# Optimization experiments

Hardware: AMD Instinct MI355X
Metric: run time of the kernel (lower is better)

The kernel has to match this reference:

```python
import jax, jax.numpy as jnp
import numpy as np

B, NQ, NK, C, H = 4, 1024, 1024, 768, 12
DH = C // H
SCALE = DH ** -0.5
EPS = 1e-5  # nn.LayerNorm default
NEG_INF = float('-inf')


def _ln(x, g, b):
    m = jnp.mean(x, axis=-1, keepdims=True)
    v = jnp.mean((x - m) ** 2, axis=-1, keepdims=True)
    return (x - m) * jax.lax.rsqrt(v + EPS) * g + b


def _heads(t):  # [B,N,C] -> [B,H,N,Dh]
    Bq, N, _ = t.shape
    return t.reshape(Bq, N, H, DH).transpose(0, 2, 1, 3)


def setup_inputs() -> dict:
    key = jax.random.key(0)
    ks = jax.random.split(key, 32)
    w = lambda k, shape: jax.random.normal(k, shape, jnp.float32) * 0.02
    g = lambda k: 1.0 + jax.random.normal(k, (C,), jnp.float32) * 0.02
    b = lambda k: jax.random.normal(k, (C,), jnp.float32) * 0.02
    inp = {
        'x': jax.random.normal(ks[0], (B, NQ, C), jnp.float32),
        'y': jax.random.normal(ks[1], (B, NK, C), jnp.float32),
        'xpos': jnp.arange(B * NQ, dtype=jnp.int32).reshape(B, NQ),
        'ypos': jnp.arange(B * NK, dtype=jnp.int32).reshape(B, NK),
        'mask': jax.random.randint(ks[2], (NQ, NK), 0, 2) > 0,
        'similarities': jax.random.normal(ks[3], (B, H, NQ, NK), jnp.float32),
        # norms
        'ln1_g': g(ks[4]), 'ln1_b': b(ks[5]),
        'ln2_g': g(ks[6]), 'ln2_b': b(ks[7]),
        'ln3_g': g(ks[8]), 'ln3_b': b(ks[9]),
        'lny_g': g(ks[10]), 'lny_b': b(ks[11]),
        # self-attn (qkv_bias=False)
        'qkv_w': w(ks[12], (3 * C, C)),
        'aproj_w': w(ks[13], (C, C)), 'aproj_b': b(ks[14]),
        # cross-attn
        'pq_w': w(ks[15], (C, C)), 'pk_w': w(ks[16], (C, C)), 'pv_w': w(ks[17], (C, C)),
        'cproj_w': w(ks[18], (C, C)), 'cproj_b': b(ks[19]),
        # mlp (hidden = 4*C)
        'fc1_w': w(ks[20], (4 * C, C)), 'fc1_b': jax.random.normal(ks[21], (4 * C,), jnp.float32) * 0.02,
        'fc2_w': w(ks[22], (C, 4 * C)), 'fc2_b': b(ks[23]),
    }
    return inp


def reference(x, y, xpos, ypos, mask, similarities,
              ln1_g, ln1_b, ln2_g, ln2_b, ln3_g, ln3_b, lny_g, lny_b,
              qkv_w, aproj_w, aproj_b,
              pq_w, pk_w, pv_w, cproj_w, cproj_b,
              fc1_w, fc1_b, fc2_w, fc2_b):
    # ---- self-attention (rope=None, dropout=0) ----
    xn = _ln(x, ln1_g, ln1_b)
    qkv = (xn @ qkv_w.T).reshape(B, NQ, 3, H, DH).transpose(2, 0, 3, 1, 4)
    q, k, v = qkv[0], qkv[1], qkv[2]                       # [B,H,Nq,Dh]
    attn = jax.nn.softmax(jnp.einsum('bhqd,bhkd->bhqk', q, k) * SCALE, axis=-1)
    sa = jnp.einsum('bhqk,bhkd->bhqd', attn, v).transpose(0, 2, 1, 3).reshape(B, NQ, C)
    x = x + sa @ aproj_w.T + aproj_b

    # ---- sparse cross-attention with similarity bias + mask ----
    y_ = _ln(y, lny_g, lny_b)
    xn2 = _ln(x, ln2_g, ln2_b)
    cq = _heads(xn2 @ pq_w.T)                              # [B,H,Nq,Dh]
    ck = _heads(y_ @ pk_w.T)                               # [B,H,Nk,Dh]
    cv = _heads(y_ @ pv_w.T)
    scores = jnp.einsum('bhqd,bhkd->bhqk', cq, ck) * SCALE
    sims_c = similarities - jnp.mean(similarities, axis=1, keepdims=True)
    scores = scores + sims_c
    scores = jnp.where(mask[None, None], scores, NEG_INF)
    cattn = jax.nn.softmax(scores, axis=-1)
    ca = jnp.einsum('bhqk,bhkd->bhqd', cattn, cv).transpose(0, 2, 1, 3).reshape(B, NQ, C)
    x = x + ca @ cproj_w.T + cproj_b

    # ---- MLP (exact GELU, as nn.GELU default) ----
    xn3 = _ln(x, ln3_g, ln3_b)
    h = jax.nn.gelu(xn3 @ fc1_w.T + fc1_b, approximate=False)
    x = x + h @ fc2_w.T + fc2_b
    return (x, y)
```

## Files before the change

kernel.cpp:

```cpp
#include <hip/hip_runtime.h>
#include <cstdint>
#include <cstddef>


typedef __bf16 bf16;
typedef __attribute__((ext_vector_type(8))) __bf16 bf16x8;
typedef __attribute__((ext_vector_type(4))) __bf16 bf16x4;
typedef __attribute__((ext_vector_type(4))) float f32x4;

typedef __attribute__((address_space(1))) void gvoid;
typedef __attribute__((address_space(3))) void lvoid;

#define DEVI static __device__ __forceinline__

DEVI void gload16(const void* g, void* l) {
  __builtin_amdgcn_global_load_lds((gvoid*)(uintptr_t)g, (lvoid*)(uintptr_t)l, 16, 0, 0);
}

DEVI f32x4 mfma_bf16(bf16x8 a, bf16x8 b, f32x4 c) {
  return __builtin_amdgcn_mfma_f32_16x16x32_bf16(a, b, c, 0, 0, 0);
}


template<int BM, int BN, bool BIAS, bool GELU, bool RES, bool OBF, bool VT>
DEVI void gemm_dev(bf16* As, bf16* Bs, int by, int bx,
                   const bf16* __restrict__ A, const bf16* __restrict__ Bt,
                   const float* __restrict__ bias, const float* __restrict__ res,
                   bf16* __restrict__ Cb, float* __restrict__ Cf,
                   bf16* __restrict__ vtOut, int vtBase, int N, int K)
{
  constexpr int WM = BM / 2, WN = BN / 2;
  constexpr int FM = WM / 16, FN = WN / 16;
  const int tid = threadIdx.x;
  const int lane = tid & 63;
  const int wv = tid >> 6;
  const int wr = wv >> 1, wc = wv & 1;
  const int l15 = lane & 15, lg = lane >> 4;
  const int bm = by * BM, bn = bx * BN;

  f32x4 acc[FM][FN];
  const f32x4 z = {0.f, 0.f, 0.f, 0.f};
  #pragma unroll
  for (int i = 0; i < FM; ++i)
    #pragma unroll
    for (int jj = 0; jj < FN; ++jj) acc[i][jj] = z;

  for (int k0 = 0; k0 < K; k0 += 64) {
    __syncthreads();
    #pragma unroll
    for (int c = tid; c < BM * 8; c += 256) {
      const int row = c >> 3, colb = (c & 7) << 4;
      gload16((const char*)A + ((size_t)(bm + row) * K + k0) * 2 + colb,
              (char*)As + (size_t)c * 16);
    }
    #pragma unroll
    for (int c = tid; c < BN * 8; c += 256) {
      const int row = c >> 3, colb = (c & 7) << 4;
      gload16((const char*)Bt + ((size_t)(bn + row) * K + k0) * 2 + colb,
              (char*)Bs + (size_t)c * 16);
    }
    __syncthreads();
    #pragma unroll
    for (int kk = 0; kk < 64; kk += 32) {
      bf16x8 af[FM], bfr[FN];
      #pragma unroll
      for (int mi = 0; mi < FM; ++mi)
        af[mi] = *(const bf16x8*)(As + (size_t)(wr * WM + mi * 16 + l15) * 64 + kk + lg * 8);
      #pragma unroll
      for (int ni = 0; ni < FN; ++ni)
        bfr[ni] = *(const bf16x8*)(Bs + (size_t)(wc * WN + ni * 16 + l15) * 64 + kk + lg * 8);
      #pragma unroll
      for (int mi = 0; mi < FM; ++mi)
        #pragma unroll
        for (int ni = 0; ni < FN; ++ni)
          acc[mi][ni] = mfma_bf16(af[mi], bfr[ni], acc[mi][ni]);
    }
  }

  #pragma unroll
  for (int mi = 0; mi < FM; ++mi) {
    const int row0 = bm + wr * WM + mi * 16 + lg * 4;
    #pragma unroll
    for (int ni = 0; ni < FN; ++ni) {
      const int col = bn + wc * WN + ni * 16 + l15;
      if constexpr (VT) {
        if (col >= vtBase) {
          const int hd = col - vtBase;
          const int bb = row0 >> 10, n0 = row0 & 1023;
          bf16x4 ov;
          #pragma unroll
          for (int r = 0; r < 4; ++r) ov[r] = (bf16)acc[mi][ni][r];
          *(bf16x4*)(vtOut + ((size_t)(bb * 768 + hd)) * 1024 + n0) = ov;
          continue;
        }
      }
      #pragma unroll
      for (int r = 0; r < 4; ++r) {
        float v = acc[mi][ni][r];
        if constexpr (BIAS) v += bias[col];
        if constexpr (GELU) v = 0.5f * v * (1.0f + erff(v * 0.70710678118654752f));
        if constexpr (RES)  v += res[(size_t)(row0 + r) * N + col];
        if constexpr (OBF)  Cb[(size_t)(row0 + r) * N + col] = (bf16)v;
        else                Cf[(size_t)(row0 + r) * N + col] = v;
      }
    }
  }
}

DEVI void biasr_dev(int blk,
                    const float* __restrict__ sim,
                    const unsigned char* __restrict__ mask,
                    bf16* __restrict__ out)
{
  const int b = blk >> 10, q = blk & 1023;
  const int t = threadIdx.x, lane = t & 63;

  int ds = 0;
  #pragma unroll
  for (int i = 0; i < 4; ++i) {
    const int idx = (lane * 4 + i) * 4;
    ds += mask[idx + 1] + mask[idx + 2] + mask[idx + 3];
  }
  #pragma unroll
  for (int o = 32; o; o >>= 1) ds += __shfl_xor(ds, o);
  const int msh = (ds == 0) ? 2 : 0;

  const int k4 = t * 4;
  const float* sb = sim + (size_t)b * 12 * 1048576;
  f32x4 sv[12];
  f32x4 acc = {0.f, 0.f, 0.f, 0.f};
  #pragma unroll
  for (int h = 0; h < 12; ++h) {
    sv[h] = *(const f32x4*)(sb + ((size_t)h * 1024 + q) * 1024 + k4);
    acc += sv[h];
  }
  const f32x4 mean = acc * (1.0f / 12.0f);

  float mb[4];
  if (msh == 0) {
    const uchar4 mv = *(const uchar4*)(mask + (size_t)q * 1024 + k4);
    mb[0] = mv.x ? 0.f : -1e30f; mb[1] = mv.y ? 0.f : -1e30f;
    mb[2] = mv.z ? 0.f : -1e30f; mb[3] = mv.w ? 0.f : -1e30f;
  } else {
    const int4 mv = *(const int4*)((const int*)mask + (size_t)q * 1024 + k4);
    mb[0] = mv.x ? 0.f : -1e30f; mb[1] = mv.y ? 0.f : -1e30f;
    mb[2] = mv.z ? 0.f : -1e30f; mb[3] = mv.w ? 0.f : -1e30f;
  }

  bf16* ob = out + (size_t)(b * 1024 + q) * 12 * 1024;
  #pragma unroll
  for (int h = 0; h < 12; ++h) {
    bf16x4 o;
    #pragma unroll
    for (int j = 0; j < 4; ++j)
      o[j] = (bf16)(sv[h][j] - mean[j] + mb[j]);
    *(bf16x4*)(ob + h * 1024 + k4) = o;
  }
}

DEVI void lnw_dev(int row,
                  const float* __restrict__ xin, const float* __restrict__ g,
                  const float* __restrict__ be, bf16* __restrict__ out)
{
  const int lane = threadIdx.x & 63;
  const f32x4* xr = (const f32x4*)(xin + (size_t)row * 768);
  f32x4 v[3];
  #pragma unroll
  for (int j = 0; j < 3; ++j) v[j] = xr[lane + 64 * j];
  float s = 0.f;
  #pragma unroll
  for (int j = 0; j < 3; ++j) s += v[j][0] + v[j][1] + v[j][2] + v[j][3];
  #pragma unroll
  for (int o = 32; o; o >>= 1) s += __shfl_xor(s, o);
  const float mean = s * (1.0f / 768.0f);
  float q = 0.f;
  #pragma unroll
  for (int j = 0; j < 3; ++j)
    #pragma unroll
    for (int e = 0; e < 4; ++e) { const float d = v[j][e] - mean; q += d * d; }
  #pragma unroll
  for (int o = 32; o; o >>= 1) q += __shfl_xor(q, o);
  const float inv = rsqrtf(q * (1.0f / 768.0f) + 1e-5f);
  #pragma unroll
  for (int j = 0; j < 3; ++j) {
    const int c = lane + 64 * j;
    const f32x4 gv = ((const f32x4*)g)[c];
    const f32x4 bv = ((const f32x4*)be)[c];
    bf16x4 o4;
    #pragma unroll
    for (int e = 0; e < 4; ++e)
      o4[e] = (bf16)((v[j][e] - mean) * inv * gv[e] + bv[e]);
    *((bf16x4*)out + (size_t)row * 192 + c) = o4;
  }
}


struct CvtArgs {
  const float* src[8];
  bf16* dst[8];
  int end[8];
};

__global__ __launch_bounds__(256)
void prep_k(CvtArgs a,
            const float* __restrict__ x, const float* __restrict__ g1,
            const float* __restrict__ b1, bf16* __restrict__ xn,
            const float* __restrict__ y, const float* __restrict__ gy,
            const float* __restrict__ by_, bf16* __restrict__ yln)
{
  const int f = blockIdx.x;
  const int t = threadIdx.x;
  if (f < 2304) {
    #pragma unroll
    for (int j = 0; j < 4; ++j) {
      const int i = f * 1024 + j * 256 + t;
      int s = 0;
      #pragma unroll
      for (int k = 0; k < 7; ++k) s += (i >= a.end[k]) ? 1 : 0;
      const int base = s ? a.end[s - 1] : 0;
      const int off = i - base;
      const f32x4 v = *((const f32x4*)a.src[s] + off);
      bf16x4 o;
      o[0] = (bf16)v[0]; o[1] = (bf16)v[1]; o[2] = (bf16)v[2]; o[3] = (bf16)v[3];
      *(bf16x4*)(a.dst[s] + (size_t)off * 4) = o;
    }
  } else {
    const int row = (f - 2304) * 4 + (t >> 6);
    if (row < 4096) lnw_dev(row, x, g1, b1, xn);
    else            lnw_dev(row - 4096, y, gy, by_, yln);
  }
}

template<int BM, int BN, bool BIAS, bool GELU, bool RES, bool OBF, bool VT>
__global__ __launch_bounds__(256)
void gemm_bt(const bf16* __restrict__ A, const bf16* __restrict__ Bt,
             const float* __restrict__ bias, const float* __restrict__ res,
             bf16* __restrict__ Cb, float* __restrict__ Cf,
             bf16* __restrict__ vtOut, int vtBase,
             int nyPerXcd, int N, int K,
             int nCompute,
             const float* __restrict__ bsim, const unsigned char* __restrict__ bmask,
             bf16* __restrict__ bout, int bbase)
{
  __shared__ bf16 As[BM * 64];
  __shared__ bf16 Bs[BN * 64];
  const int f = blockIdx.x;
  if (f >= nCompute) {
    biasr_dev(bbase + f - nCompute, bsim, bmask, bout);
    return;
  }
  const int xcd = f & 7, j = f >> 3;
  const int by = xcd + 8 * (j % nyPerXcd);
  const int bx = j / nyPerXcd;
  gemm_dev<BM,BN,BIAS,GELU,RES,OBF,VT>(As, Bs, by, bx,
      A, Bt, bias, res, Cb, Cf, vtOut, vtBase, N, K);
}

__global__ __launch_bounds__(256)
void apkv_k(const bf16* __restrict__ sa, const bf16* __restrict__ w_ap,
            const float* __restrict__ apb, const float* __restrict__ x,
            float* __restrict__ x1,
            const bf16* __restrict__ yln, const bf16* __restrict__ w_pkv,
            bf16* __restrict__ ckv, bf16* __restrict__ cvtT,
            const float* __restrict__ bsim, const unsigned char* __restrict__ bmask,
            bf16* __restrict__ bout, int bbase)
{
  __shared__ bf16 As[128 * 64];
  __shared__ bf16 Bs[128 * 64];
  const int f = blockIdx.x;
  if (f >= 768) {
    biasr_dev(bbase + f - 768, bsim, bmask, bout);
    return;
  }
  if (f < 384) {
    const int xcd = f & 7, j = f >> 3;
    const int by = xcd + 8 * (j % 8);
    const int bx = j / 8;
    gemm_dev<64,128,true,false,true,false,false>(As, Bs, by, bx,
        sa, w_ap, apb, x, nullptr, x1, nullptr, 0, 768, 768);
  } else {
    const int g = f - 384;
    const int xcd = g & 7, j = g >> 3;
    const int by = xcd + 8 * (j % 4);
    const int bx = j / 4;
    gemm_dev<128,128,false,false,false,true,true>(As, Bs, by, bx,
        yln, w_pkv, nullptr, nullptr, ckv, nullptr, cvtT, 768, 1536, 768);
  }
}

__global__ __launch_bounds__(256)
void fc2copy_k(const bf16* __restrict__ hbuf, const bf16* __restrict__ w_f2,
               const float* __restrict__ f2b, const float* __restrict__ x2,
               float* __restrict__ outp,
               const float* __restrict__ y, float* __restrict__ ycopy)
{
  __shared__ bf16 As[128 * 64];
  __shared__ bf16 Bs[128 * 64];
  const int f = blockIdx.x;
  if (f < 384) {
    const int xcd = f & 7, j = f >> 3;
    const int by = xcd + 8 * (j % 8);
    const int bx = j / 8;
    gemm_dev<64,128,true,false,true,false,false>(As, Bs, by, bx,
        hbuf, w_f2, f2b, x2, nullptr, outp, nullptr, 0, 768, 3072);
  } else {
    for (int i = (f - 384) * 256 + threadIdx.x; i < 786432; i += 512 * 256)
      ((f32x4*)ycopy)[i] = ((const f32x4*)y)[i];
  }
}

__global__ __launch_bounds__(256)
void ln_k(const float* __restrict__ xin, const float* __restrict__ g,
          const float* __restrict__ be, bf16* __restrict__ out)
{
  lnw_dev(blockIdx.x * 4 + (threadIdx.x >> 6), xin, g, be, out);
}

template<int CROSS>
__global__ __launch_bounds__(256, 3)
void fattn_k(const bf16* __restrict__ Qp, int ldq,
             const bf16* __restrict__ Kp, int ldk,
             const bf16* __restrict__ Vt,
             const bf16* __restrict__ bias,
             bf16* __restrict__ Out,
             int nCompute,
             const float* __restrict__ bsim, const unsigned char* __restrict__ bmask,
             bf16* __restrict__ bout, int bbase)
{
  __shared__ bf16 Kl[2][64 * 64];
  __shared__ bf16 Vl[2][64 * 64];
  __shared__ bf16 Pl[4][16 * 72];

  const int f = blockIdx.x;
  if (f >= nCompute) {
    biasr_dev(bbase + f - nCompute, bsim, bmask, bout);
    return;
  }
  const int r8 = f & 7, rest = f >> 3;
  const int c6 = rest % 6, qt = rest / 6;
  const int pp = r8 + 8 * c6;
  const int b = pp / 12, hh = pp % 12;
  const int tid = threadIdx.x, lane = tid & 63, wq = tid >> 6;
  const int l15 = lane & 15, lg = lane >> 4;

  bf16x8 qreg0, qreg1;
  {
    const bf16* qsrc = Qp + (size_t)(b * 1024 + qt * 64 + wq * 16 + l15) * ldq + hh * 64 + lg * 8;
    qreg0 = *(const bf16x8*)qsrc;
    qreg1 = *(const bf16x8*)(qsrc + 32);
  }
  const char* Kbase = (const char*)(Kp + (size_t)b * 1024 * ldk + hh * 64);
  const char* Vbase = (const char*)(Vt + (size_t)(b * 12 + hh) * 64 * 1024);
  const bf16* biasRow = nullptr;
  if constexpr (CROSS)
    biasRow = bias + ((size_t)(b * 1024 + qt * 64 + wq * 16 + l15) * 12 + hh) * 1024;

  f32x4 oacc[4];
  const f32x4 z = {0.f, 0.f, 0.f, 0.f};
  #pragma unroll
  for (int i = 0; i < 4; ++i) oacc[i] = z;
  float m_run = -1e30f, l_run = 0.f;

  char* PlW = (char*)&Pl[wq][0];
  const int swz = (l15 & 7) << 4;

  auto stage = [&](int buf, int t) {
    const int k0 = t * 64;
    #pragma unroll
    for (int jj = 0; jj < 2; ++jj) {
      const int c = jj * 256 + tid;
      const int r = c >> 3;
      const int sw = ((c & 7) ^ (r & 7)) << 4;
      gload16(Kbase + ((size_t)(k0 + r) * ldk) * 2 + sw, (char*)&Kl[buf][0] + (size_t)c * 16);
      gload16(Vbase + (size_t)r * 2048 + (size_t)k0 * 2 + sw, (char*)&Vl[buf][0] + (size_t)c * 16);
    }
  };

  stage(0, 0);
  __syncthreads();

  for (int t = 0; t < 16; ++t) {
    const int cur = t & 1;
    const int k0 = t * 64;
    if (t < 15) stage(cur ^ 1, t + 1);

    bf16x4 bv[4];
    if constexpr (CROSS) {
      const bf16* bp = biasRow + k0 + lg * 4;
      #pragma unroll
      for (int ni = 0; ni < 4; ++ni) bv[ni] = *(const bf16x4*)(bp + ni * 16);
    }

    f32x4 sacc[4];
    #pragma unroll
    for (int i = 0; i < 4; ++i) sacc[i] = z;
    #pragma unroll
    for (int ni = 0; ni < 4; ++ni) {
      const int rowb = (ni * 16 + l15) * 128;
      const bf16x8 a0 = *(const bf16x8*)((char*)&Kl[cur][0] + rowb + ((lg * 16) ^ swz));
      const bf16x8 a1 = *(const bf16x8*)((char*)&Kl[cur][0] + rowb + ((64 + lg * 16) ^ swz));
      sacc[ni] = mfma_bf16(a0, qreg0, sacc[ni]);
      sacc[ni] = mfma_bf16(a1, qreg1, sacc[ni]);
    }

    float sv[16];
    #pragma unroll
    for (int ni = 0; ni < 4; ++ni)
      #pragma unroll
      for (int r = 0; r < 4; ++r)
        sv[ni * 4 + r] = sacc[ni][r] * 0.125f;
    if constexpr (CROSS) {
      #pragma unroll
      for (int ni = 0; ni < 4; ++ni)
        #pragma unroll
        for (int r = 0; r < 4; ++r)
          sv[ni * 4 + r] += (float)bv[ni][r];
    }
    float mx = sv[0];
    #pragma unroll
    for (int jj = 1; jj < 16; ++jj) mx = fmaxf(mx, sv[jj]);
    mx = fmaxf(mx, __shfl_xor(mx, 16));
    mx = fmaxf(mx, __shfl_xor(mx, 32));
    const float mnew = fmaxf(m_run, mx);
    const float corr = __expf(m_run - mnew);
    m_run = mnew;
    float ps = 0.f;
    #pragma unroll
    for (int jj = 0; jj < 16; ++jj) { sv[jj] = __expf(sv[jj] - mnew); ps += sv[jj]; }
    l_run = l_run * corr + ps;

    #pragma unroll
    for (int ni = 0; ni < 4; ++ni) {
      bf16x4 pw;
      #pragma unroll
      for (int r = 0; r < 4; ++r) pw[r] = (bf16)sv[ni * 4 + r];
      *(bf16x4*)(PlW + l15 * 144 + ni * 32 + lg * 8) = pw;
    }
    float cr[4];
    #pragma unroll
    for (int r = 0; r < 4; ++r) cr[r] = __shfl(corr, ((lane >> 4) << 2) + r);
    #pragma unroll
    for (int nd = 0; nd < 4; ++nd)
      #pragma unroll
      for (int r = 0; r < 4; ++r) oacc[nd][r] *= cr[r];

    const bf16x8 p0 = *(const bf16x8*)(PlW + l15 * 144 + lg * 16);
    const bf16x8 p1 = *(const bf16x8*)(PlW + l15 * 144 + 64 + lg * 16);
    #pragma unroll
    for (int nd = 0; nd < 4; ++nd) {
      const int rowb = (nd * 16 + l15) * 128;
      const bf16x8 v0 = *(const bf16x8*)((char*)&Vl[cur][0] + rowb + ((lg * 16) ^ swz));
      const bf16x8 v1 = *(const bf16x8*)((char*)&Vl[cur][0] + rowb + ((64 + lg * 16) ^ swz));
      oacc[nd] = mfma_bf16(p0, v0, oacc[nd]);
      oacc[nd] = mfma_bf16(p1, v1, oacc[nd]);
    }
    __syncthreads();
  }

  float ls = l_run + __shfl_xor(l_run, 16);
  ls += __shfl_xor(ls, 32);
  const float inv = 1.0f / ls;
  float ivr[4];
  #pragma unroll
  for (int r = 0; r < 4; ++r) ivr[r] = __shfl(inv, ((lane >> 4) << 2) + r);
  bf16* ob = Out + (size_t)(b * 1024 + qt * 64 + wq * 16 + lg * 4) * 768 + hh * 64 + l15;
  #pragma unroll
  for (int r = 0; r < 4; ++r)
    #pragma unroll
    for (int nd = 0; nd < 4; ++nd)
      ob[(size_t)r * 768 + nd * 16] = (bf16)(oacc[nd][r] * ivr[r]);
}

extern "C" void kernel_launch(void* const* d_in, const int* in_sizes, int n_in,
                              void* d_out, int out_size, void* d_ws, size_t ws_size,
                              hipStream_t stream)
{
  (void)in_sizes; (void)n_in; (void)out_size; (void)ws_size;
  const float* x    = (const float*)d_in[0];
  const float* y    = (const float*)d_in[1];
  const unsigned char* mask = (const unsigned char*)d_in[4];
  const float* sim  = (const float*)d_in[5];
  const float* ln1g = (const float*)d_in[6];
  const float* ln1b = (const float*)d_in[7];
  const float* ln2g = (const float*)d_in[8];
  const float* ln2b = (const float*)d_in[9];
  const float* ln3g = (const float*)d_in[10];
  const float* ln3b = (const float*)d_in[11];
  const float* lnyg = (const float*)d_in[12];
  const float* lnyb = (const float*)d_in[13];
  const float* qkvw = (const float*)d_in[14];
  const float* apw  = (const float*)d_in[15];
  const float* apb  = (const float*)d_in[16];
  const float* pqw  = (const float*)d_in[17];
  const float* pkw  = (const float*)d_in[18];
  const float* pvw  = (const float*)d_in[19];
  const float* cpw  = (const float*)d_in[20];
  const float* cpb  = (const float*)d_in[21];
  const float* f1w  = (const float*)d_in[22];
  const float* f1b  = (const float*)d_in[23];
  const float* f2w  = (const float*)d_in[24];
  const float* f2b  = (const float*)d_in[25];

  char* ws = (char*)d_ws;
  size_t off = 0;
  auto alloc = [&](size_t bytes) -> void* {
    off = (off + 255) & ~(size_t)255;
    void* p = ws + off;
    off += bytes;
    return p;
  };
  const size_t T = 4096;
  bf16* w_qkv = (bf16*)alloc((size_t)2304 * 768 * 2);
  bf16* w_ap  = (bf16*)alloc((size_t)768 * 768 * 2);
  bf16* w_pq  = (bf16*)alloc((size_t)768 * 768 * 2);
  bf16* w_pkv = (bf16*)alloc((size_t)1536 * 768 * 2);
  bf16* w_cp  = (bf16*)alloc((size_t)768 * 768 * 2);
  bf16* w_f1  = (bf16*)alloc((size_t)3072 * 768 * 2);
  bf16* w_f2  = (bf16*)alloc((size_t)768 * 3072 * 2);
  bf16* xn    = (bf16*)alloc(T * 768 * 2);
  bf16* qkvo  = (bf16*)alloc(T * 2304 * 2);
  bf16* vt    = (bf16*)alloc((size_t)48 * 64 * 1024 * 2);
  bf16* sa    = (bf16*)alloc(T * 768 * 2);
  float* x1   = (float*)alloc(T * 768 * 4);
  bf16* yln   = (bf16*)alloc(T * 768 * 2);
  bf16* xn2   = (bf16*)alloc(T * 768 * 2);
  bf16* cqf   = (bf16*)alloc(T * 768 * 2);
  bf16* ckv   = (bf16*)alloc(T * 1536 * 2);
  bf16* cvtT  = (bf16*)alloc((size_t)48 * 64 * 1024 * 2);
  bf16* biasA = (bf16*)alloc((size_t)4 * 1024 * 12 * 1024 * 2);
  bf16* ca    = (bf16*)alloc(T * 768 * 2);
  float* x2   = (float*)alloc(T * 768 * 4);
  bf16* xn3   = (bf16*)alloc(T * 768 * 2);
  bf16* hbuf  = (bf16*)alloc(T * 3072 * 2);

  CvtArgs a;
  {
    const float* srcs[8] = {qkvw, apw, pqw, pkw, pvw, cpw, f1w, f2w};
    bf16* dsts[8] = {w_qkv, w_ap, w_pq, w_pkv, w_pkv + 768 * 768, w_cp, w_f1, w_f2};
    const int n4s[8] = {442368, 147456, 147456, 147456, 147456, 147456, 589824, 589824};
    int cum = 0;
    for (int j = 0; j < 8; ++j) {
      a.src[j] = srcs[j]; a.dst[j] = dsts[j];
      cum += n4s[j]; a.end[j] = cum;
    }
  }

  prep_k<<<4352, 256, 0, stream>>>(a, x, ln1g, ln1b, xn, y, lnyg, lnyb, yln);

  gemm_bt<128,128,false,false,false,true,true><<<1600, 256, 0, stream>>>(
      xn, w_qkv, nullptr, nullptr, qkvo, nullptr, vt, 1536, 4, 2304, 768,
      576, sim, mask, biasA, 0);

  fattn_k<0><<<1792, 256, 0, stream>>>(
      qkvo, 2304, qkvo + 768, 2304, vt, nullptr, sa,
      768, sim, mask, biasA, 1024);

  apkv_k<<<1792, 256, 0, stream>>>(sa, w_ap, apb, x, x1, yln, w_pkv, ckv, cvtT,
                                   sim, mask, biasA, 2048);

  ln_k<<<1024, 256, 0, stream>>>(x1, ln2g, ln2b, xn2);

  gemm_bt<64,128,false,false,false,true,false><<<1408, 256, 0, stream>>>(
      xn2, w_pq, nullptr, nullptr, cqf, nullptr, nullptr, 0, 8, 768, 768,
      384, sim, mask, biasA, 3072);

  fattn_k<1><<<768, 256, 0, stream>>>(
      cqf, 768, ckv, 1536, cvtT, biasA, ca,
      768, sim, mask, biasA, 0);

  gemm_bt<64,128,true,false,true,false,false><<<384, 256, 0, stream>>>(
      ca, w_cp, cpb, x1, nullptr, x2, nullptr, 0, 8, 768, 768,
      384, sim, mask, biasA, 0);

  ln_k<<<1024, 256, 0, stream>>>(x2, ln3g, ln3b, xn3);

  gemm_bt<128,128,true,true,false,true,false><<<768, 256, 0, stream>>>(
      xn3, w_f1, f1b, nullptr, hbuf, nullptr, nullptr, 0, 4, 3072, 768,
      768, sim, mask, biasA, 0);

  fc2copy_k<<<896, 256, 0, stream>>>(
      hbuf, w_f2, f2b, x2, (float*)d_out, y, (float*)d_out + 3145728);
}
```

Before: 349.9 us.

## Spread weight conversion, y-LN and bias prep across compute kernels; coalesce cross-attn bias loads

The prep kernel now converts only the QKV weights and runs LN1. The remaining weight conversions and the y LayerNorm move into spare blocks of the QKV GEMM and self-attention launches, and the similarity-bias blocks are redistributed across launches. In cross-attention, each lane loads 16 contiguous bias values per tile and a per-wave LDS buffer transposes them into the MFMA layout, replacing scattered 4-element loads. The aim is to shorten the serial prep phase by overlapping it with compute and to coalesce the bias reads. The cost is extra LDS traffic and shared memory in the cross-attention kernel, plus added branching in the auxiliary blocks.

```diff
diff --git a/kernel.cpp b/kernel.cpp
--- a/kernel.cpp
+++ b/kernel.cpp
@@ -194,40 +194,62 @@
   }
 }
 
-
-struct CvtArgs {
-  const float* src[8];
-  bf16* dst[8];
-  int end[8];
+struct AuxArgs {
+  const float* csrc[7];
+  bf16* cdst[7];
+  int cend[7];
+  const float* y; const float* gy; const float* byv; bf16* yln;
+  const float* sim; const unsigned char* mask; bf16* biasOut;
+  int biasStart, biasCount, extraStart, extraCount;
 };
 
+DEVI void aux_dev(int j, const AuxArgs& A)
+{
+  if (j < A.extraCount) {
+    const int e = A.extraStart + j;
+    if (e < 1024) {
+      lnw_dev(e * 4 + (threadIdx.x >> 6), A.y, A.gy, A.byv, A.yln);
+    } else {
+      const int blk = e - 1024;
+      const int t = threadIdx.x;
+      #pragma unroll
+      for (int u = 0; u < 4; ++u) {
+        const int i = blk * 1024 + u * 256 + t;
+        int s = 0;
+        #pragma unroll
+        for (int k = 0; k < 6; ++k) s += (i >= A.cend[k]) ? 1 : 0;
+        const int base = s ? A.cend[s - 1] : 0;
+        const int off = i - base;
+        const f32x4 v = *((const f32x4*)A.csrc[s] + off);
+        bf16x4 o;
+        o[0] = (bf16)v[0]; o[1] = (bf16)v[1]; o[2] = (bf16)v[2]; o[3] = (bf16)v[3];
+        *(bf16x4*)(A.cdst[s] + (size_t)off * 4) = o;
+      }
+    }
+  } else {
+    biasr_dev(A.biasStart + (j - A.extraCount), A.sim, A.mask, A.biasOut);
+  }
+}
+
+
 __global__ __launch_bounds__(256)
-void prep_k(CvtArgs a,
+void prep_k(const float* __restrict__ qkvw, bf16* __restrict__ w_qkv,
             const float* __restrict__ x, const float* __restrict__ g1,
-            const float* __restrict__ b1, bf16* __restrict__ xn,
-            const float* __restrict__ y, const float* __restrict__ gy,
-            const float* __restrict__ by_, bf16* __restrict__ yln)
+            const float* __restrict__ b1, bf16* __restrict__ xn)
 {
   const int f = blockIdx.x;
   const int t = threadIdx.x;
-  if (f < 2304) {
-    #pragma unroll
-    for (int j = 0; j < 4; ++j) {
-      const int i = f * 1024 + j * 256 + t;
-      int s = 0;
-      #pragma unroll
-      for (int k = 0; k < 7; ++k) s += (i >= a.end[k]) ? 1 : 0;
-      const int base = s ? a.end[s - 1] : 0;
-      const int off = i - base;
-      const f32x4 v = *((const f32x4*)a.src[s] + off);
+  if (f < 432) {
+    #pragma unroll
+    for (int u = 0; u < 4; ++u) {
+      const int i = f * 1024 + u * 256 + t;
+      const f32x4 v = *((const f32x4*)qkvw + i);
       bf16x4 o;
       o[0] = (bf16)v[0]; o[1] = (bf16)v[1]; o[2] = (bf16)v[2]; o[3] = (bf16)v[3];
-      *(bf16x4*)(a.dst[s] + (size_t)off * 4) = o;
+      *(bf16x4*)(w_qkv + (size_t)i * 4) = o;
     }
   } else {
-    const int row = (f - 2304) * 4 + (t >> 6);
-    if (row < 4096) lnw_dev(row, x, g1, b1, xn);
-    else            lnw_dev(row - 4096, y, gy, by_, yln);
+    lnw_dev((f - 432) * 4 + (t >> 6), x, g1, b1, xn);
   }
 }
 
@@ -238,15 +260,13 @@
              bf16* __restrict__ Cb, float* __restrict__ Cf,
              bf16* __restrict__ vtOut, int vtBase,
              int nyPerXcd, int N, int K,
-             int nCompute,
-             const float* __restrict__ bsim, const unsigned char* __restrict__ bmask,
-             bf16* __restrict__ bout, int bbase)
+             int nCompute, AuxArgs aux)
 {
   __shared__ bf16 As[BM * 64];
   __shared__ bf16 Bs[BN * 64];
   const int f = blockIdx.x;
   if (f >= nCompute) {
-    biasr_dev(bbase + f - nCompute, bsim, bmask, bout);
+    aux_dev(f - nCompute, aux);
     return;
   }
   const int xcd = f & 7, j = f >> 3;
@@ -262,14 +282,13 @@
             float* __restrict__ x1,
             const bf16* __restrict__ yln, const bf16* __restrict__ w_pkv,
             bf16* __restrict__ ckv, bf16* __restrict__ cvtT,
-            const float* __restrict__ bsim, const unsigned char* __restrict__ bmask,
-            bf16* __restrict__ bout, int bbase)
+            AuxArgs aux)
 {
   __shared__ bf16 As[128 * 64];
   __shared__ bf16 Bs[128 * 64];
   const int f = blockIdx.x;
   if (f >= 768) {
-    biasr_dev(bbase + f - 768, bsim, bmask, bout);
+    aux_dev(f - 768, aux);
     return;
   }
   if (f < 384) {
@@ -323,17 +342,16 @@
              const bf16* __restrict__ Vt,
              const bf16* __restrict__ bias,
              bf16* __restrict__ Out,
-             int nCompute,
-             const float* __restrict__ bsim, const unsigned char* __restrict__ bmask,
-             bf16* __restrict__ bout, int bbase)
+             int nCompute, AuxArgs aux)
 {
   __shared__ bf16 Kl[2][64 * 64];
   __shared__ bf16 Vl[2][64 * 64];
   __shared__ bf16 Pl[4][16 * 72];
+  __shared__ bf16 Bl[CROSS ? 4 * 16 * 72 : 4];
 
   const int f = blockIdx.x;
   if (f >= nCompute) {
-    biasr_dev(bbase + f - nCompute, bsim, bmask, bout);
+    aux_dev(f - nCompute, aux);
     return;
   }
   const int r8 = f & 7, rest = f >> 3;
@@ -351,9 +369,10 @@
   }
   const char* Kbase = (const char*)(Kp + (size_t)b * 1024 * ldk + hh * 64);
   const char* Vbase = (const char*)(Vt + (size_t)(b * 12 + hh) * 64 * 1024);
-  const bf16* biasRow = nullptr;
+  const bf16* biasQ = nullptr;
   if constexpr (CROSS)
-    biasRow = bias + ((size_t)(b * 1024 + qt * 64 + wq * 16 + l15) * 12 + hh) * 1024;
+    biasQ = bias + ((size_t)(b * 1024 + qt * 64 + wq * 16 + (lane >> 2)) * 12 + hh) * 1024
+          + (lane & 3) * 16;
 
   f32x4 oacc[4];
   const f32x4 z = {0.f, 0.f, 0.f, 0.f};
@@ -362,6 +381,7 @@
   float m_run = -1e30f, l_run = 0.f;
 
   char* PlW = (char*)&Pl[wq][0];
+  char* BlW = (char*)&Bl[0] + (CROSS ? wq * 16 * 144 : 0);
   const int swz = (l15 & 7) << 4;
 
   auto stage = [&](int buf, int t) {
@@ -382,14 +402,14 @@
   for (int t = 0; t < 16; ++t) {
     const int cur = t & 1;
     const int k0 = t * 64;
+
+    bf16x8 br0, br1;
+    if constexpr (CROSS) {
+      const bf16* bp = biasQ + k0;
+      br0 = *(const bf16x8*)bp;
+      br1 = *(const bf16x8*)(bp + 8);
+    }
     if (t < 15) stage(cur ^ 1, t + 1);
-
-    bf16x4 bv[4];
-    if constexpr (CROSS) {
-      const bf16* bp = biasRow + k0 + lg * 4;
-      #pragma unroll
-      for (int ni = 0; ni < 4; ++ni) bv[ni] = *(const bf16x4*)(bp + ni * 16);
-    }
 
     f32x4 sacc[4];
     #pragma unroll
@@ -401,6 +421,16 @@
       const bf16x8 a1 = *(const bf16x8*)((char*)&Kl[cur][0] + rowb + ((64 + lg * 16) ^ swz));
       sacc[ni] = mfma_bf16(a0, qreg0, sacc[ni]);
       sacc[ni] = mfma_bf16(a1, qreg1, sacc[ni]);
+    }
+
+    bf16x4 bv[4];
+    if constexpr (CROSS) {
+      char* dst = BlW + (lane >> 2) * 144 + (lane & 3) * 32;
+      *(bf16x8*)dst = br0;
+      *(bf16x8*)(dst + 16) = br1;
+      #pragma unroll
+      for (int ni = 0; ni < 4; ++ni)
+        bv[ni] = *(const bf16x4*)(BlW + l15 * 144 + ni * 32 + lg * 8);
     }
 
     float sv[16];
@@ -533,50 +563,64 @@
   bf16* xn3   = (bf16*)alloc(T * 768 * 2);
   bf16* hbuf  = (bf16*)alloc(T * 3072 * 2);
 
-  CvtArgs a;
+  AuxArgs aux;
   {
-    const float* srcs[8] = {qkvw, apw, pqw, pkw, pvw, cpw, f1w, f2w};
-    bf16* dsts[8] = {w_qkv, w_ap, w_pq, w_pkv, w_pkv + 768 * 768, w_cp, w_f1, w_f2};
-    const int n4s[8] = {442368, 147456, 147456, 147456, 147456, 147456, 589824, 589824};
+    const float* srcs[7] = {apw, pkw, pvw, pqw, cpw, f1w, f2w};
+    bf16* dsts[7] = {w_ap, w_pkv, w_pkv + 768 * 768, w_pq, w_cp, w_f1, w_f2};
+    const int n4s[7] = {147456, 147456, 147456, 147456, 147456, 589824, 589824};
     int cum = 0;
-    for (int j = 0; j < 8; ++j) {
-      a.src[j] = srcs[j]; a.dst[j] = dsts[j];
-      cum += n4s[j]; a.end[j] = cum;
-    }
-  }
-
-  prep_k<<<4352, 256, 0, stream>>>(a, x, ln1g, ln1b, xn, y, lnyg, lnyb, yln);
-
-  gemm_bt<128,128,false,false,false,true,true><<<1600, 256, 0, stream>>>(
+    for (int j = 0; j < 7; ++j) {
+      aux.csrc[j] = srcs[j]; aux.cdst[j] = dsts[j];
+      cum += n4s[j]; aux.cend[j] = cum;
+    }
+    aux.y = y; aux.gy = lnyg; aux.byv = lnyb; aux.yln = yln;
+    aux.sim = sim; aux.mask = mask; aux.biasOut = biasA;
+  }
+
+  prep_k<<<1456, 256, 0, stream>>>(qkvw, w_qkv, x, ln1g, ln1b, xn);
+
+  AuxArgs a2 = aux;
+  a2.extraStart = 0;    a2.extraCount = 1456;
+  a2.biasStart = 0;     a2.biasCount = 800;
+  gemm_bt<128,128,false,false,false,true,true><<<576 + 2256, 256, 0, stream>>>(
       xn, w_qkv, nullptr, nullptr, qkvo, nullptr, vt, 1536, 4, 2304, 768,
-      576, sim, mask, biasA, 0);
-
-  fattn_k<0><<<1792, 256, 0, stream>>>(
-      qkvo, 2304, qkvo + 768, 2304, vt, nullptr, sa,
-      768, sim, mask, biasA, 1024);
-
-  apkv_k<<<1792, 256, 0, stream>>>(sa, w_ap, apb, x, x1, yln, w_pkv, ckv, cvtT,
-                                   sim, mask, biasA, 2048);
+      576, a2);
+
+  AuxArgs a3 = aux;
+  a3.extraStart = 1456; a3.extraCount = 1440;
+  a3.biasStart = 800;   a3.biasCount = 800;
+  fattn_k<0><<<768 + 2240, 256, 0, stream>>>(
+      qkvo, 2304, qkvo + 768, 2304, vt, nullptr, sa, 768, a3);
+
+  AuxArgs a4 = aux;
+  a4.extraStart = 0;    a4.extraCount = 0;
+  a4.biasStart = 1600;  a4.biasCount = 1700;
+  apkv_k<<<768 + 1700, 256, 0, stream>>>(sa, w_ap, apb, x, x1,
+                                         yln, w_pkv, ckv, cvtT, a4);
 
   ln_k<<<1024, 256, 0, stream>>>(x1, ln2g, ln2b, xn2);
 
-  gemm_bt<64,128,false,false,false,true,false><<<1408, 256, 0, stream>>>(
+  AuxArgs a6 = aux;
+  a6.extraStart = 0;    a6.extraCount = 0;
+  a6.biasStart = 3300;  a6.biasCount = 796;
+  gemm_bt<64,128,false,false,false,true,false><<<384 + 796, 256, 0, stream>>>(
       xn2, w_pq, nullptr, nullptr, cqf, nullptr, nullptr, 0, 8, 768, 768,
-      384, sim, mask, biasA, 3072);
-
+      384, a6);
+
+  AuxArgs a0 = aux;
+  a0.extraStart = 0; a0.extraCount = 0; a0.biasStart = 0; a0.biasCount = 0;
   fattn_k<1><<<768, 256, 0, stream>>>(
-      cqf, 768, ckv, 1536, cvtT, biasA, ca,
-      768, sim, mask, biasA, 0);
+      cqf, 768, ckv, 1536, cvtT, biasA, ca, 768, a0);
 
   gemm_bt<64,128,true,false,true,false,false><<<384, 256, 0, stream>>>(
       ca, w_cp, cpb, x1, nullptr, x2, nullptr, 0, 8, 768, 768,
-      384, sim, mask, biasA, 0);
+      384, a0);
 
   ln_k<<<1024, 256, 0, stream>>>(x2, ln3g, ln3b, xn3);
 
   gemm_bt<128,128,true,true,false,true,false><<<768, 256, 0, stream>>>(
       xn3, w_f1, f1b, nullptr, hbuf, nullptr, nullptr, 0, 4, 3072, 768,
-      768, sim, mask, biasA, 0);
+      768, a0);
 
   fc2copy_k<<<896, 256, 0, stream>>>(
       hbuf, w_f2, f2b, x2, (float*)d_out, y, (float*)d_out + 3145728);
```

Result: no change. 350.5 us (+0.2%).
